# Optimization experiments

Measured on AMD Instinct MI355X. Metric: run time of the kernel, lower is better.

## Reference

```python
import jax, jax.numpy as jnp
import numpy as np

B, T, I, H = 256, 2048, 10, 64  # batch, frames, features_len, hidden_size (8*8)


def setup_inputs() -> dict:
    key = jax.random.key(0)
    k1, k2, k3, k4, k5 = jax.random.split(key, 5)
    s = 1.0 / np.sqrt(H)  # PyTorch GRU init scale
    noise = jax.random.normal(k1, (B, T, I), dtype=jnp.float32)
    w_ih = jax.random.uniform(k2, (3 * H, I), minval=-s, maxval=s, dtype=jnp.float32)
    w_hh = jax.random.uniform(k3, (3 * H, H), minval=-s, maxval=s, dtype=jnp.float32)
    b_ih = jax.random.uniform(k4, (3 * H,), minval=-s, maxval=s, dtype=jnp.float32)
    b_hh = jax.random.uniform(k5, (3 * H,), minval=-s, maxval=s, dtype=jnp.float32)
    return {"noise": noise, "w_ih": w_ih, "w_hh": w_hh, "b_ih": b_ih, "b_hh": b_hh}


def reference(noise, w_ih, w_hh, b_ih, b_hh):
    # Single-layer batch_first GRU, PyTorch gate ordering (r, z, n).
    b, t, _ = noise.shape
    h_dim = w_hh.shape[1]
    # Input projections for all timesteps at once: (B, T, 3H)
    gi = jnp.einsum('bti,gi->btg', noise, w_ih) + b_ih
    w_hr, w_hz, w_hn = jnp.split(w_hh, 3, axis=0)
    b_hr, b_hz, b_hn = jnp.split(b_hh, 3)

    def step(h, g):
        g_r, g_z, g_n = jnp.split(g, 3, axis=-1)
        r = jax.nn.sigmoid(g_r + h @ w_hr.T + b_hr)
        z = jax.nn.sigmoid(g_z + h @ w_hz.T + b_hz)
        n = jnp.tanh(g_n + r * (h @ w_hn.T + b_hn))
        h_new = (1.0 - z) * n + z * h
        return h_new, h_new

    h0 = jnp.zeros((b, h_dim), dtype=noise.dtype)
    _, out_t = jax.lax.scan(step, h0, jnp.swapaxes(gi, 0, 1))  # (T, B, H)
    return jnp.swapaxes(out_t, 0, 1)  # (B, T, H)
```

## Files before the change

kernel.cpp:

```cpp
#include <hip/hip_runtime.h>


#define Bn 256
#define Tn 2048
#define In 10
#define Hn 64

typedef _Float16 h2 __attribute__((ext_vector_type(2)));

__device__ __forceinline__ float dot2(h2 a, h2 b, float c) {
    return __builtin_amdgcn_fdot2(a, b, c, false);
}

extern "C" __global__
__attribute__((amdgpu_flat_work_group_size(128, 128), amdgpu_waves_per_eu(1, 1)))
void gru_kernel(
    const float* __restrict__ noise,
    const float* __restrict__ w_ih,
    const float* __restrict__ w_hh,
    const float* __restrict__ b_ih,
    const float* __restrict__ b_hh,
    float* __restrict__ out)
{
    const int b   = blockIdx.x;
    const int tid = threadIdx.x;
    const int u   = ((tid >> 6) << 5) | (tid & 31);
    const int kh  = (tid >> 5) & 1;

    __shared__ alignas(16) unsigned short xbuf[Tn * 12];
    __shared__ alignas(16) unsigned short hbuf[2][Hn];

    {
        const float* xp = noise + (size_t)b * Tn * In;
        for (int c = 0; c < Tn / 128; ++c) {
            const int t = c * 128 + tid;
            const float* px = xp + (size_t)t * In;
            float v[In];
#pragma unroll
            for (int i = 0; i < In; i += 2) {
                float2 f = *(const float2*)(px + i);
                v[i] = f.x; v[i + 1] = f.y;
            }
            unsigned int p[5];
#pragma unroll
            for (int i = 0; i < 5; ++i)
                p[i] = __builtin_bit_cast(unsigned int,
                           h2{(_Float16)v[2 * i], (_Float16)v[2 * i + 1]});
            unsigned int* xw = (unsigned int*)(xbuf + t * 12);
            *(uint2*)(xw + 0) = uint2{p[0], p[1]};
            *(uint2*)(xw + 2) = uint2{p[2], p[3]};
            xw[4] = p[4];
        }
        if (tid < Hn) { hbuf[0][tid] = 0; hbuf[1][tid] = 0; }
    }

    const float SR = -1.44269504f;
    const float SN =  2.88539008f;

    h2 wr[16], wz[16], wn[16];
    {
        const float* pr = w_hh + (size_t)(0 * Hn + u) * Hn + kh * 32;
        const float* pz = w_hh + (size_t)(1 * Hn + u) * Hn + kh * 32;
        const float* pn = w_hh + (size_t)(2 * Hn + u) * Hn + kh * 32;
#pragma unroll
        for (int k = 0; k < 16; ++k) {
            wr[k] = h2{(_Float16)(SR * pr[2 * k]), (_Float16)(SR * pr[2 * k + 1])};
            wz[k] = h2{(_Float16)(SR * pz[2 * k]), (_Float16)(SR * pz[2 * k + 1])};
            wn[k] = h2{(_Float16)(SN * pn[2 * k]), (_Float16)(SN * pn[2 * k + 1])};
        }
    }
    float wir[In], wiz[In], win[In];
#pragma unroll
    for (int i = 0; i < In; ++i) {
        wir[i] = SR * w_ih[(0 * Hn + u) * In + i];
        wiz[i] = SR * w_ih[(1 * Hn + u) * In + i];
        win[i] = SN * w_ih[(2 * Hn + u) * In + i];
    }
    const float brz_r = SR * (b_ih[0 * Hn + u] + b_hh[0 * Hn + u]);
    const float brz_z = SR * (b_ih[1 * Hn + u] + b_hh[1 * Hn + u]);
    const float bi_n  = SN * b_ih[2 * Hn + u];
    const float bh_n0 = ((tid & 63) < 32) ? SN * b_hh[2 * Hn + u] : 0.0f;

#pragma unroll
    for (int k = 0; k < 16; ++k)
        asm volatile("" : "+v"(wr[k]), "+v"(wz[k]), "+v"(wn[k]));
#pragma unroll
    for (int i = 0; i < In; ++i)
        asm volatile("" : "+v"(wir[i]), "+v"(wiz[i]), "+v"(win[i]));

    float hold = 0.0f;
    float* __restrict__ op = out + (size_t)b * Tn * Hn;

    __syncthreads();

    for (int t = 0; t < Tn; ++t) {
        const unsigned int* xr = (const unsigned int*)(xbuf + t * 12);
        uint2 xa  = *(const uint2*)(xr + 0);
        uint2 xb2 = *(const uint2*)(xr + 2);
        unsigned int xc4 = xr[4];

        const uint4* hq4 = (const uint4*)(&hbuf[t & 1][kh * 32]);
        uint4 q0 = hq4[0], q1 = hq4[1], q2 = hq4[2], q3 = hq4[3];

        float xf[10];
        {
            h2 t0 = __builtin_bit_cast(h2, xa.x),  t1 = __builtin_bit_cast(h2, xa.y);
            h2 t2 = __builtin_bit_cast(h2, xb2.x), t3 = __builtin_bit_cast(h2, xb2.y);
            h2 t4 = __builtin_bit_cast(h2, xc4);
            xf[0] = (float)t0[0]; xf[1] = (float)t0[1];
            xf[2] = (float)t1[0]; xf[3] = (float)t1[1];
            xf[4] = (float)t2[0]; xf[5] = (float)t2[1];
            xf[6] = (float)t3[0]; xf[7] = (float)t3[1];
            xf[8] = (float)t4[0]; xf[9] = (float)t4[1];
        }
        float gr = brz_r, gz = brz_z, gn = bi_n;
#pragma unroll
        for (int i = 0; i < In; ++i) {
            gr = fmaf(wir[i], xf[i], gr);
            gz = fmaf(wiz[i], xf[i], gz);
            gn = fmaf(win[i], xf[i], gn);
        }

        float ar0 = 0.f, ar1 = 0.f, az0 = 0.f, az1 = 0.f, an0 = bh_n0, an1 = 0.f;
#pragma unroll
        for (int q = 0; q < 4; ++q) {
            uint4 uq = (q == 0) ? q0 : (q == 1) ? q1 : (q == 2) ? q2 : q3;
            h2 p0 = __builtin_bit_cast(h2, uq.x);
            h2 p1 = __builtin_bit_cast(h2, uq.y);
            h2 p2 = __builtin_bit_cast(h2, uq.z);
            h2 p3 = __builtin_bit_cast(h2, uq.w);
            const int k = 4 * q;
            ar0 = dot2(wr[k + 0], p0, ar0); az0 = dot2(wz[k + 0], p0, az0); an0 = dot2(wn[k + 0], p0, an0);
            ar1 = dot2(wr[k + 1], p1, ar1); az1 = dot2(wz[k + 1], p1, az1); an1 = dot2(wn[k + 1], p1, an1);
            ar0 = dot2(wr[k + 2], p2, ar0); az0 = dot2(wz[k + 2], p2, az0); an0 = dot2(wn[k + 2], p2, an0);
            ar1 = dot2(wr[k + 3], p3, ar1); az1 = dot2(wz[k + 3], p3, az1); an1 = dot2(wn[k + 3], p3, an1);
        }
        float ar = ar0 + ar1, az = az0 + az1, an = an0 + an1;
        ar += __shfl_xor(ar, 32);
        az += __shfl_xor(az, 32);
        an += __shfl_xor(an, 32);

        const float r  = __builtin_amdgcn_rcpf(1.0f + __builtin_amdgcn_exp2f(gr + ar));
        const float z  = __builtin_amdgcn_rcpf(1.0f + __builtin_amdgcn_exp2f(gz + az));
        const float pn2 = fmaf(r, an, gn);
        const float e   = __builtin_amdgcn_exp2f(pn2);
        const float nn  = fmaf(-2.0f, __builtin_amdgcn_rcpf(e + 1.0f), 1.0f);
        const float hn  = fmaf(z, hold - nn, nn);
        hold = hn;

        if ((tid & 63) < 32) {
            op[(size_t)t * Hn + u] = hn;
            hbuf[(t + 1) & 1][u] =
                __builtin_bit_cast(unsigned short, (_Float16)hn);
        }
        __syncthreads();
    }
}

extern "C" void kernel_launch(void* const* d_in, const int* in_sizes, int n_in,
                              void* d_out, int out_size, void* d_ws, size_t ws_size,
                              hipStream_t stream) {
    gru_kernel<<<Bn, 128, 0, stream>>>(
        (const float*)d_in[0], (const float*)d_in[1], (const float*)d_in[2],
        (const float*)d_in[3], (const float*)d_in[4], (float*)d_out);
}
```

Measured before the change: 858.1 us.

## Run each GRU batch row in one wavefront, removing barriers and shuffle reductions

Shrinks the block from two wavefronts to one 64-lane wavefront. Each lane now owns a full hidden unit and computes the whole 64-wide recurrent dot product, so the cross-half shuffle reduction and the per-step __syncthreads are gone. The hidden-state buffer becomes single-buffered, relying on the wave's in-order LDS accesses. The next step's input features are also prefetched from LDS a step ahead. In exchange, each lane does twice the dot2 work per step and holds twice as many recurrent weight registers, which lengthens the serial per-step ALU path.

```diff
diff --git a/kernel.cpp b/kernel.cpp
--- a/kernel.cpp
+++ b/kernel.cpp
@@ -13,7 +13,7 @@
 }
 
 extern "C" __global__
-__attribute__((amdgpu_flat_work_group_size(128, 128), amdgpu_waves_per_eu(1, 1)))
+__attribute__((amdgpu_flat_work_group_size(64, 64), amdgpu_waves_per_eu(1, 1)))
 void gru_kernel(
     const float* __restrict__ noise,
     const float* __restrict__ w_ih,
@@ -22,18 +22,16 @@
     const float* __restrict__ b_hh,
     float* __restrict__ out)
 {
-    const int b   = blockIdx.x;
-    const int tid = threadIdx.x;
-    const int u   = ((tid >> 6) << 5) | (tid & 31);
-    const int kh  = (tid >> 5) & 1;
+    const int b = blockIdx.x;
+    const int j = threadIdx.x;
 
     __shared__ alignas(16) unsigned short xbuf[Tn * 12];
-    __shared__ alignas(16) unsigned short hbuf[2][Hn];
+    __shared__ alignas(16) unsigned short hbuf[Hn];
 
     {
         const float* xp = noise + (size_t)b * Tn * In;
-        for (int c = 0; c < Tn / 128; ++c) {
-            const int t = c * 128 + tid;
+        for (int c = 0; c < Tn / 64; ++c) {
+            const int t = c * 64 + j;
             const float* px = xp + (size_t)t * In;
             float v[In];
 #pragma unroll
@@ -51,19 +49,19 @@
             *(uint2*)(xw + 2) = uint2{p[2], p[3]};
             xw[4] = p[4];
         }
-        if (tid < Hn) { hbuf[0][tid] = 0; hbuf[1][tid] = 0; }
+        hbuf[j] = 0;
     }
 
     const float SR = -1.44269504f;
     const float SN =  2.88539008f;
 
-    h2 wr[16], wz[16], wn[16];
+    h2 wr[32], wz[32], wn[32];
     {
-        const float* pr = w_hh + (size_t)(0 * Hn + u) * Hn + kh * 32;
-        const float* pz = w_hh + (size_t)(1 * Hn + u) * Hn + kh * 32;
-        const float* pn = w_hh + (size_t)(2 * Hn + u) * Hn + kh * 32;
+        const float* pr = w_hh + (size_t)(0 * Hn + j) * Hn;
+        const float* pz = w_hh + (size_t)(1 * Hn + j) * Hn;
+        const float* pn = w_hh + (size_t)(2 * Hn + j) * Hn;
 #pragma unroll
-        for (int k = 0; k < 16; ++k) {
+        for (int k = 0; k < 32; ++k) {
             wr[k] = h2{(_Float16)(SR * pr[2 * k]), (_Float16)(SR * pr[2 * k + 1])};
             wz[k] = h2{(_Float16)(SR * pz[2 * k]), (_Float16)(SR * pz[2 * k + 1])};
             wn[k] = h2{(_Float16)(SN * pn[2 * k]), (_Float16)(SN * pn[2 * k + 1])};
@@ -72,17 +70,17 @@
     float wir[In], wiz[In], win[In];
 #pragma unroll
     for (int i = 0; i < In; ++i) {
-        wir[i] = SR * w_ih[(0 * Hn + u) * In + i];
-        wiz[i] = SR * w_ih[(1 * Hn + u) * In + i];
-        win[i] = SN * w_ih[(2 * Hn + u) * In + i];
+        wir[i] = SR * w_ih[(0 * Hn + j) * In + i];
+        wiz[i] = SR * w_ih[(1 * Hn + j) * In + i];
+        win[i] = SN * w_ih[(2 * Hn + j) * In + i];
     }
-    const float brz_r = SR * (b_ih[0 * Hn + u] + b_hh[0 * Hn + u]);
-    const float brz_z = SR * (b_ih[1 * Hn + u] + b_hh[1 * Hn + u]);
-    const float bi_n  = SN * b_ih[2 * Hn + u];
-    const float bh_n0 = ((tid & 63) < 32) ? SN * b_hh[2 * Hn + u] : 0.0f;
+    const float brz_r = SR * (b_ih[0 * Hn + j] + b_hh[0 * Hn + j]);
+    const float brz_z = SR * (b_ih[1 * Hn + j] + b_hh[1 * Hn + j]);
+    const float bi_n  = SN * b_ih[2 * Hn + j];
+    const float bh_n  = SN * b_hh[2 * Hn + j];
 
 #pragma unroll
-    for (int k = 0; k < 16; ++k)
+    for (int k = 0; k < 32; ++k)
         asm volatile("" : "+v"(wr[k]), "+v"(wz[k]), "+v"(wn[k]));
 #pragma unroll
     for (int i = 0; i < In; ++i)
@@ -91,21 +89,32 @@
     float hold = 0.0f;
     float* __restrict__ op = out + (size_t)b * Tn * Hn;
 
-    __syncthreads();
+    unsigned int xc0, xc1, xc2, xc3, xc4;
+    {
+        const unsigned int* xr = (const unsigned int*)xbuf;
+        uint2 a = *(const uint2*)(xr + 0);
+        uint2 c = *(const uint2*)(xr + 2);
+        xc0 = a.x; xc1 = a.y; xc2 = c.x; xc3 = c.y; xc4 = xr[4];
+    }
 
     for (int t = 0; t < Tn; ++t) {
-        const unsigned int* xr = (const unsigned int*)(xbuf + t * 12);
-        uint2 xa  = *(const uint2*)(xr + 0);
-        uint2 xb2 = *(const uint2*)(xr + 2);
-        unsigned int xc4 = xr[4];
+        const uint4* hq4 = (const uint4*)hbuf;
+        uint4 q0 = hq4[0], q1 = hq4[1], q2 = hq4[2], q3 = hq4[3];
+        uint4 q4 = hq4[4], q5 = hq4[5], q6 = hq4[6], q7 = hq4[7];
 
-        const uint4* hq4 = (const uint4*)(&hbuf[t & 1][kh * 32]);
-        uint4 q0 = hq4[0], q1 = hq4[1], q2 = hq4[2], q3 = hq4[3];
+        unsigned int xn0, xn1, xn2, xn3, xn4;
+        {
+            const int tn = (t + 1 < Tn) ? (t + 1) : t;
+            const unsigned int* xr = (const unsigned int*)(xbuf + tn * 12);
+            uint2 a = *(const uint2*)(xr + 0);
+            uint2 c = *(const uint2*)(xr + 2);
+            xn0 = a.x; xn1 = a.y; xn2 = c.x; xn3 = c.y; xn4 = xr[4];
+        }
 
-        float xf[10];
+        float xf[In];
         {
-            h2 t0 = __builtin_bit_cast(h2, xa.x),  t1 = __builtin_bit_cast(h2, xa.y);
-            h2 t2 = __builtin_bit_cast(h2, xb2.x), t3 = __builtin_bit_cast(h2, xb2.y);
+            h2 t0 = __builtin_bit_cast(h2, xc0), t1 = __builtin_bit_cast(h2, xc1);
+            h2 t2 = __builtin_bit_cast(h2, xc2), t3 = __builtin_bit_cast(h2, xc3);
             h2 t4 = __builtin_bit_cast(h2, xc4);
             xf[0] = (float)t0[0]; xf[1] = (float)t0[1];
             xf[2] = (float)t1[0]; xf[3] = (float)t1[1];
@@ -121,10 +130,11 @@
             gn = fmaf(win[i], xf[i], gn);
         }
 
-        float ar0 = 0.f, ar1 = 0.f, az0 = 0.f, az1 = 0.f, an0 = bh_n0, an1 = 0.f;
+        float ar0 = 0.f, ar1 = 0.f, az0 = 0.f, az1 = 0.f, an0 = bh_n, an1 = 0.f;
 #pragma unroll
-        for (int q = 0; q < 4; ++q) {
-            uint4 uq = (q == 0) ? q0 : (q == 1) ? q1 : (q == 2) ? q2 : q3;
+        for (int q = 0; q < 8; ++q) {
+            uint4 uq = (q == 0) ? q0 : (q == 1) ? q1 : (q == 2) ? q2 : (q == 3) ? q3
+                     : (q == 4) ? q4 : (q == 5) ? q5 : (q == 6) ? q6 : q7;
             h2 p0 = __builtin_bit_cast(h2, uq.x);
             h2 p1 = __builtin_bit_cast(h2, uq.y);
             h2 p2 = __builtin_bit_cast(h2, uq.z);
@@ -135,32 +145,30 @@
             ar0 = dot2(wr[k + 2], p2, ar0); az0 = dot2(wz[k + 2], p2, az0); an0 = dot2(wn[k + 2], p2, an0);
             ar1 = dot2(wr[k + 3], p3, ar1); az1 = dot2(wz[k + 3], p3, az1); an1 = dot2(wn[k + 3], p3, an1);
         }
-        float ar = ar0 + ar1, az = az0 + az1, an = an0 + an1;
-        ar += __shfl_xor(ar, 32);
-        az += __shfl_xor(az, 32);
-        an += __shfl_xor(an, 32);
+        const float ar = ar0 + ar1;
+        const float az = az0 + az1;
+        const float an = an0 + an1;
 
-        const float r  = __builtin_amdgcn_rcpf(1.0f + __builtin_amdgcn_exp2f(gr + ar));
-        const float z  = __builtin_amdgcn_rcpf(1.0f + __builtin_amdgcn_exp2f(gz + az));
+        const float r   = __builtin_amdgcn_rcpf(1.0f + __builtin_amdgcn_exp2f(gr + ar));
+        const float z   = __builtin_amdgcn_rcpf(1.0f + __builtin_amdgcn_exp2f(gz + az));
         const float pn2 = fmaf(r, an, gn);
         const float e   = __builtin_amdgcn_exp2f(pn2);
         const float nn  = fmaf(-2.0f, __builtin_amdgcn_rcpf(e + 1.0f), 1.0f);
         const float hn  = fmaf(z, hold - nn, nn);
         hold = hn;
 
-        if ((tid & 63) < 32) {
-            op[(size_t)t * Hn + u] = hn;
-            hbuf[(t + 1) & 1][u] =
-                __builtin_bit_cast(unsigned short, (_Float16)hn);
-        }
-        __syncthreads();
+        op[(size_t)t * Hn + j] = hn;
+
+        hbuf[j] = __builtin_bit_cast(unsigned short, (_Float16)hn);
+
+        xc0 = xn0; xc1 = xn1; xc2 = xn2; xc3 = xn3; xc4 = xn4;
     }
 }
 
 extern "C" void kernel_launch(void* const* d_in, const int* in_sizes, int n_in,
                               void* d_out, int out_size, void* d_ws, size_t ws_size,
                               hipStream_t stream) {
-    gru_kernel<<<Bn, 128, 0, stream>>>(
+    gru_kernel<<<Bn, 64, 0, stream>>>(
         (const float*)d_in[0], (const float*)d_in[1], (const float*)d_in[2],
         (const float*)d_in[3], (const float*)d_in[4], (float*)d_out);
 }
```

Result: slower. 892.5 us (+4.0%).

## Interleave K-halves across adjacent lanes, stage inputs as fp32, use raw barrier

Applied to the files above, without the earlier changes.

Remaps threads so the two K-halves of each hidden unit sit on adjacent lanes, making the cross-half reduction a lane-xor-1 shuffle (DPP-friendly) instead of xor-32. Stores the input sequence in shared memory as fp32, removing the per-step half-to-float conversions at the cost of twice the LDS footprint (96KB). Replaces __syncthreads with an explicit lgkmcnt wait plus s_barrier and unrolls the time loop by 2. The lighter barrier skips the vmcnt wait on global output stores, which shortens the serial per-step critical path.

```diff
diff --git a/kernel.cpp b/kernel.cpp
--- a/kernel.cpp
+++ b/kernel.cpp
@@ -24,32 +24,29 @@
 {
     const int b   = blockIdx.x;
     const int tid = threadIdx.x;
-    const int u   = ((tid >> 6) << 5) | (tid & 31);
-    const int kh  = (tid >> 5) & 1;
+    const int wv  = tid >> 6;
+    const int l   = tid & 63;
+    const int u   = wv * 32 + (l >> 1);
+    const int kh  = l & 1;
 
-    __shared__ alignas(16) unsigned short xbuf[Tn * 12];
+    __shared__ alignas(16) float xs[Tn][12];
     __shared__ alignas(16) unsigned short hbuf[2][Hn];
 
     {
         const float* xp = noise + (size_t)b * Tn * In;
-        for (int c = 0; c < Tn / 128; ++c) {
-            const int t = c * 128 + tid;
-            const float* px = xp + (size_t)t * In;
-            float v[In];
-#pragma unroll
-            for (int i = 0; i < In; i += 2) {
-                float2 f = *(const float2*)(px + i);
-                v[i] = f.x; v[i + 1] = f.y;
-            }
-            unsigned int p[5];
-#pragma unroll
-            for (int i = 0; i < 5; ++i)
-                p[i] = __builtin_bit_cast(unsigned int,
-                           h2{(_Float16)v[2 * i], (_Float16)v[2 * i + 1]});
-            unsigned int* xw = (unsigned int*)(xbuf + t * 12);
-            *(uint2*)(xw + 0) = uint2{p[0], p[1]};
-            *(uint2*)(xw + 2) = uint2{p[2], p[3]};
-            xw[4] = p[4];
+        for (int r = tid; r < Tn; r += 128) {
+            const float* px = xp + (size_t)r * In;
+            float2 a0 = *(const float2*)(px + 0);
+            float2 a1 = *(const float2*)(px + 2);
+            float2 a2 = *(const float2*)(px + 4);
+            float2 a3 = *(const float2*)(px + 6);
+            float2 a4 = *(const float2*)(px + 8);
+            float* d = xs[r];
+            *(float2*)(d + 0) = a0;
+            *(float2*)(d + 2) = a1;
+            *(float2*)(d + 4) = a2;
+            *(float2*)(d + 6) = a3;
+            *(float2*)(d + 8) = a4;
         }
         if (tid < Hn) { hbuf[0][tid] = 0; hbuf[1][tid] = 0; }
     }
@@ -79,7 +76,7 @@
     const float brz_r = SR * (b_ih[0 * Hn + u] + b_hh[0 * Hn + u]);
     const float brz_z = SR * (b_ih[1 * Hn + u] + b_hh[1 * Hn + u]);
     const float bi_n  = SN * b_ih[2 * Hn + u];
-    const float bh_n0 = ((tid & 63) < 32) ? SN * b_hh[2 * Hn + u] : 0.0f;
+    const float bh_n0 = (kh == 0) ? SN * b_hh[2 * Hn + u] : 0.0f;
 
 #pragma unroll
     for (int k = 0; k < 16; ++k)
@@ -93,33 +90,27 @@
 
     __syncthreads();
 
+#pragma unroll 2
     for (int t = 0; t < Tn; ++t) {
-        const unsigned int* xr = (const unsigned int*)(xbuf + t * 12);
-        uint2 xa  = *(const uint2*)(xr + 0);
-        uint2 xb2 = *(const uint2*)(xr + 2);
-        unsigned int xc4 = xr[4];
+        const float* xr = xs[t];
+        float4 xA = *(const float4*)(xr + 0);
+        float4 xB = *(const float4*)(xr + 4);
+        float2 xC = *(const float2*)(xr + 8);
 
-        const uint4* hq4 = (const uint4*)(&hbuf[t & 1][kh * 32]);
-        uint4 q0 = hq4[0], q1 = hq4[1], q2 = hq4[2], q3 = hq4[3];
+        const uint4* hq = (const uint4*)(&hbuf[t & 1][kh * 32]);
+        uint4 q0 = hq[0], q1 = hq[1], q2 = hq[2], q3 = hq[3];
 
-        float xf[10];
-        {
-            h2 t0 = __builtin_bit_cast(h2, xa.x),  t1 = __builtin_bit_cast(h2, xa.y);
-            h2 t2 = __builtin_bit_cast(h2, xb2.x), t3 = __builtin_bit_cast(h2, xb2.y);
-            h2 t4 = __builtin_bit_cast(h2, xc4);
-            xf[0] = (float)t0[0]; xf[1] = (float)t0[1];
-            xf[2] = (float)t1[0]; xf[3] = (float)t1[1];
-            xf[4] = (float)t2[0]; xf[5] = (float)t2[1];
-            xf[6] = (float)t3[0]; xf[7] = (float)t3[1];
-            xf[8] = (float)t4[0]; xf[9] = (float)t4[1];
-        }
         float gr = brz_r, gz = brz_z, gn = bi_n;
-#pragma unroll
-        for (int i = 0; i < In; ++i) {
-            gr = fmaf(wir[i], xf[i], gr);
-            gz = fmaf(wiz[i], xf[i], gz);
-            gn = fmaf(win[i], xf[i], gn);
-        }
+        gr = fmaf(wir[0], xA.x, gr); gz = fmaf(wiz[0], xA.x, gz); gn = fmaf(win[0], xA.x, gn);
+        gr = fmaf(wir[1], xA.y, gr); gz = fmaf(wiz[1], xA.y, gz); gn = fmaf(win[1], xA.y, gn);
+        gr = fmaf(wir[2], xA.z, gr); gz = fmaf(wiz[2], xA.z, gz); gn = fmaf(win[2], xA.z, gn);
+        gr = fmaf(wir[3], xA.w, gr); gz = fmaf(wiz[3], xA.w, gz); gn = fmaf(win[3], xA.w, gn);
+        gr = fmaf(wir[4], xB.x, gr); gz = fmaf(wiz[4], xB.x, gz); gn = fmaf(win[4], xB.x, gn);
+        gr = fmaf(wir[5], xB.y, gr); gz = fmaf(wiz[5], xB.y, gz); gn = fmaf(win[5], xB.y, gn);
+        gr = fmaf(wir[6], xB.z, gr); gz = fmaf(wiz[6], xB.z, gz); gn = fmaf(win[6], xB.z, gn);
+        gr = fmaf(wir[7], xB.w, gr); gz = fmaf(wiz[7], xB.w, gz); gn = fmaf(win[7], xB.w, gn);
+        gr = fmaf(wir[8], xC.x, gr); gz = fmaf(wiz[8], xC.x, gz); gn = fmaf(win[8], xC.x, gn);
+        gr = fmaf(wir[9], xC.y, gr); gz = fmaf(wiz[9], xC.y, gz); gn = fmaf(win[9], xC.y, gn);
 
         float ar0 = 0.f, ar1 = 0.f, az0 = 0.f, az1 = 0.f, an0 = bh_n0, an1 = 0.f;
 #pragma unroll
@@ -135,25 +126,24 @@
             ar0 = dot2(wr[k + 2], p2, ar0); az0 = dot2(wz[k + 2], p2, az0); an0 = dot2(wn[k + 2], p2, an0);
             ar1 = dot2(wr[k + 3], p3, ar1); az1 = dot2(wz[k + 3], p3, az1); an1 = dot2(wn[k + 3], p3, an1);
         }
-        float ar = ar0 + ar1, az = az0 + az1, an = an0 + an1;
-        ar += __shfl_xor(ar, 32);
-        az += __shfl_xor(az, 32);
-        an += __shfl_xor(an, 32);
+        float arp = ar0 + ar1, azp = az0 + az1, anp = an0 + an1;
+        const float ar = arp + __shfl_xor(arp, 1);
+        const float az = azp + __shfl_xor(azp, 1);
+        const float an = anp + __shfl_xor(anp, 1);
 
-        const float r  = __builtin_amdgcn_rcpf(1.0f + __builtin_amdgcn_exp2f(gr + ar));
-        const float z  = __builtin_amdgcn_rcpf(1.0f + __builtin_amdgcn_exp2f(gz + az));
+        const float r   = __builtin_amdgcn_rcpf(1.0f + __builtin_amdgcn_exp2f(gr + ar));
+        const float z   = __builtin_amdgcn_rcpf(1.0f + __builtin_amdgcn_exp2f(gz + az));
         const float pn2 = fmaf(r, an, gn);
         const float e   = __builtin_amdgcn_exp2f(pn2);
         const float nn  = fmaf(-2.0f, __builtin_amdgcn_rcpf(e + 1.0f), 1.0f);
         const float hn  = fmaf(z, hold - nn, nn);
         hold = hn;
 
-        if ((tid & 63) < 32) {
+        if (kh == 0) {
             op[(size_t)t * Hn + u] = hn;
-            hbuf[(t + 1) & 1][u] =
-                __builtin_bit_cast(unsigned short, (_Float16)hn);
+            hbuf[(t + 1) & 1][u] = __builtin_bit_cast(unsigned short, (_Float16)hn);
         }
-        __syncthreads();
+        asm volatile("s_waitcnt lgkmcnt(0)\n\ts_barrier" ::: "memory");
     }
 }
 
```

Result: faster. 830.5 us (-3.2%).
